# Performance work log

Hardware: AMD Instinct MI355X
Metric: run time of the kernel (lower is better)

## Reference

```python
import jax, jax.numpy as jnp
import numpy as np

N_ATOMS = 1_000_000
F_DIM = 128
H_DIM = 64
N_SPECIES = 4


def setup_inputs() -> dict:
    key = jax.random.key(0)
    ks = jax.random.split(key, 8)
    feats = jax.random.normal(ks[0], (N_ATOMS, F_DIM), dtype=jnp.float32)
    species = jax.random.randint(ks[1], (N_ATOMS,), 0, N_SPECIES, dtype=jnp.int64)
    # per-species MLP params, stacked on a leading species axis
    W1 = jax.random.normal(ks[2], (N_SPECIES, F_DIM, H_DIM), dtype=jnp.float32) / np.sqrt(F_DIM)
    b1 = jnp.zeros((N_SPECIES, H_DIM), dtype=jnp.float32)
    W2 = jax.random.normal(ks[3], (N_SPECIES, H_DIM, H_DIM), dtype=jnp.float32) / np.sqrt(H_DIM)
    b2 = jnp.zeros((N_SPECIES, H_DIM), dtype=jnp.float32)
    W3 = jax.random.normal(ks[4], (N_SPECIES, H_DIM, 1), dtype=jnp.float32) / np.sqrt(H_DIM)
    b3 = jnp.zeros((N_SPECIES, 1), dtype=jnp.float32)
    return {"features": feats, "species_indices": species,
            "W1": W1, "b1": b1, "W2": W2, "b2": b2, "W3": W3, "b3": b3}


def reference(features, species_indices, W1, b1, W2, b2, W3, b3):
    # Per-atom energy: dispatch each atom to its species' small tanh MLP.
    # Faithful to the torch mask-gather/scatter loop: we evaluate each
    # species MLP densely (n_species is tiny) and select per atom,
    # which computes identical outputs for the selected atoms.
    n_species = W1.shape[0]
    E = jnp.zeros((features.shape[0],), dtype=features.dtype)
    for s in range(n_species):
        h = jnp.tanh(features @ W1[s] + b1[s])   # [N, H]
        h = jnp.tanh(h @ W2[s] + b2[s])          # [N, H]
        e = (h @ W3[s] + b3[s])[:, 0]            # [N]
        E = jnp.where(species_indices == s, e, E)
    return E
```

## Files before the change

kernel.cpp:

```cpp
#include <hip/hip_runtime.h>

#define NSP 4

typedef unsigned short u16;
typedef __bf16 v8bf __attribute__((ext_vector_type(8)));
typedef float v4f __attribute__((ext_vector_type(4)));

__device__ __forceinline__ u16 f2bf(float f){
  union { float f; unsigned u; } v; v.f = f;
  unsigned u = v.u;
  u += 0x7fffu + ((u >> 16) & 1u);
  return (u16)(u >> 16);
}
__device__ __forceinline__ u16 h2bf(float f){
  union { float f; unsigned u; } v; v.f = f;
  return (u16)((v.u + 0x8000u) >> 16);
}
__device__ __forceinline__ unsigned pack2bf(float x, float y){
  union { float f; unsigned u; } a, b; a.f = x; b.f = y;
  unsigned ux = a.u + 0x8000u, uy = b.u + 0x8000u;
  return (uy & 0xffff0000u) | (ux >> 16);
}
__device__ __forceinline__ float fast_tanh(float x){
  float xc = fminf(fmaxf(x, -9.f), 9.f);
  float e = __expf(2.f * xc);
  return 1.f - 2.f * __builtin_amdgcn_rcpf(e + 1.f);
}


__global__ void init_k(int* __restrict__ counts2){
  counts2[threadIdx.x] = 0;
}

__global__ void hist_k(const int* __restrict__ sp, int n, int* __restrict__ counts2){
  int i = blockIdx.x * 256 + threadIdx.x;
  int sv = (i < n) ? sp[i] : -1;
  int b = blockIdx.x & 63;
  int lane = threadIdx.x & 63;
  #pragma unroll
  for (int s = 0; s < NSP; ++s){
    unsigned long long m = __ballot(sv == s);
    if (lane == 0 && m) atomicAdd(&counts2[s*64 + b], (int)__popcll(m));
  }
}

__global__ void scan_k(const int* __restrict__ counts2, int* __restrict__ cursors2,
                       int* __restrict__ segOff){
  __shared__ int tmp[256];
  int tid = threadIdx.x;
  int v = counts2[tid];
  tmp[tid] = v; __syncthreads();
  #pragma unroll
  for (int off = 1; off < 256; off <<= 1){
    int t = (tid >= off) ? tmp[tid - off] : 0;
    __syncthreads();
    tmp[tid] += t;
    __syncthreads();
  }
  int incl = tmp[tid];
  cursors2[tid] = incl - v;
  if ((tid & 63) == 0) segOff[tid >> 6] = incl - v;
  if (tid == 255)      segOff[NSP] = incl;
}

__global__ void scatter_k(const int* __restrict__ sp, int n,
                          int* __restrict__ cursors2, int* __restrict__ sorted){
  int i = blockIdx.x * 256 + threadIdx.x;
  int sv = (i < n) ? sp[i] : -1;
  int b = blockIdx.x & 63;
  int lane = threadIdx.x & 63;
  #pragma unroll
  for (int s = 0; s < NSP; ++s){
    unsigned long long m = __ballot(sv == s);
    if (!m) continue;
    int leader = __ffsll(m) - 1;
    int base = 0;
    if (lane == leader) base = atomicAdd(&cursors2[s*64 + b], (int)__popcll(m));
    base = __shfl(base, leader, 64);
    if (sv == s){
      int rank = (int)__popcll(m & ((1ull << lane) - 1ull));
      sorted[base + rank] = i;
    }
  }
}

__global__ void wconv_k(const float* __restrict__ W1, const float* __restrict__ W2,
                        u16* __restrict__ w1t, u16* __restrict__ w2t){
  int i = blockIdx.x * 256 + threadIdx.x;
  if (i < NSP*128*64){
    int s = i >> 13, rem = i & 8191, k = rem >> 6, nn = rem & 63;
    w1t[(s*64 + nn)*128 + k] = f2bf(W1[i]);
  }
  if (i < NSP*64*64){
    int s = i >> 12, rem = i & 4095, k = rem >> 6, nn = rem & 63;
    w2t[(s*64 + nn)*64 + k] = f2bf(W2[i]);
  }
}


#define BPS 128

__global__ __launch_bounds__(256, 2) void mlp2_k(
    const float* __restrict__ feats,
    const float* __restrict__ b1, const float* __restrict__ b2,
    const float* __restrict__ W3, const float* __restrict__ b3,
    const int* __restrict__ segOff, const int* __restrict__ sorted,
    const u16* __restrict__ w1t, const u16* __restrict__ w2t,
    float* __restrict__ out)
{
  __shared__ __align__(16) u16 sW1[64*136];
  __shared__ __align__(16) u16 sW2[64*72];
  __shared__ float sB1[64], sB2[64], sW3s[64];
  __shared__ __align__(16) u16 sH[4][16*72];

  int s  = blockIdx.x >> 7;
  int bs = blockIdx.x & (BPS-1);
  int tid = threadIdx.x;
  int segB = segOff[s], segE = segOff[s+1];
  int cnt = segE - segB;
  int tiles = (cnt + 63) >> 6;

  {
    int r = tid >> 2, q = tid & 3;
    const uint4* sp1 = (const uint4*)(w1t + (size_t)(s*64 + r)*128 + q*32);
    uint4 a0 = sp1[0], a1 = sp1[1], a2 = sp1[2], a3 = sp1[3];
    const uint4* sp2 = (const uint4*)(w2t + (size_t)(s*64 + r)*64 + q*16);
    uint4 c0 = sp2[0], c1 = sp2[1];
    uint4* d1 = (uint4*)(sW1 + r*136 + q*32);
    d1[0]=a0; d1[1]=a1; d1[2]=a2; d1[3]=a3;
    uint4* d2 = (uint4*)(sW2 + r*72 + q*16);
    d2[0]=c0; d2[1]=c1;
  }
  if (tid < 64)        sB1[tid]       = b1[s*64 + tid];
  else if (tid < 128)  sB2[tid-64]    = b2[s*64 + tid-64];
  else if (tid < 192)  sW3s[tid-128]  = W3[s*64 + tid-128];
  __syncthreads();

  int lane = tid & 63, wv = tid >> 6;
  int cc = lane & 15, quad = lane >> 4;

  v8bf bw1[4][4], bw2[4][2];
  float rb1[4], rb2[4], rw3[4];
  #pragma unroll
  for (int nt = 0; nt < 4; ++nt){
    #pragma unroll
    for (int kk = 0; kk < 4; ++kk)
      bw1[nt][kk] = *(const v8bf*)(sW1 + (nt*16+cc)*136 + kk*32 + quad*8);
    #pragma unroll
    for (int kk = 0; kk < 2; ++kk)
      bw2[nt][kk] = *(const v8bf*)(sW2 + (nt*16+cc)*72 + kk*32 + quad*8);
    rb1[nt] = sB1[nt*16+cc];
    rb2[nt] = sB2[nt*16+cc];
    rw3[nt] = sW3s[nt*16+cc];
  }
  float b3v = b3[s];
  u16* myH = sH[wv];

  if (tiles <= 0) return;

  auto idxLoad = [&](int t) -> int {
    int tc = t < tiles-1 ? t : tiles-1;
    int p = segB + tc*64 + wv*16 + cc;
    if (p > segE-1) p = segE-1;
    return sorted[p];
  };
  auto featLoad = [&](int ri, float4 (&f)[8]){
    const float4* fp = (const float4*)(feats + (size_t)ri*128 + quad*8);
    #pragma unroll
    for (int kk = 0; kk < 4; ++kk){ f[kk*2] = fp[kk*8]; f[kk*2+1] = fp[kk*8+1]; }
  };
  auto compute = [&](int t, const float4 (&f)[8], int ri){
    v4f acc[4];
    #pragma unroll
    for (int nt = 0; nt < 4; ++nt) acc[nt] = (v4f){0.f,0.f,0.f,0.f};
    #pragma unroll
    for (int kk = 0; kk < 4; ++kk){
      union { v8bf v; unsigned u[4]; } A;
      A.u[0] = pack2bf(f[kk*2].x,   f[kk*2].y);
      A.u[1] = pack2bf(f[kk*2].z,   f[kk*2].w);
      A.u[2] = pack2bf(f[kk*2+1].x, f[kk*2+1].y);
      A.u[3] = pack2bf(f[kk*2+1].z, f[kk*2+1].w);
      #pragma unroll
      for (int nt = 0; nt < 4; ++nt)
        acc[nt] = __builtin_amdgcn_mfma_f32_16x16x32_bf16(A.v, bw1[nt][kk], acc[nt], 0, 0, 0);
    }
    #pragma unroll
    for (int nt = 0; nt < 4; ++nt){
      #pragma unroll
      for (int r = 0; r < 4; ++r)
        myH[(quad*4+r)*72 + nt*16+cc] = h2bf(fast_tanh(acc[nt][r] + rb1[nt]));
    }
    v4f acc2[4];
    #pragma unroll
    for (int nt = 0; nt < 4; ++nt) acc2[nt] = (v4f){0.f,0.f,0.f,0.f};
    #pragma unroll
    for (int kk = 0; kk < 2; ++kk){
      v8bf hA = *(const v8bf*)(myH + cc*72 + kk*32 + quad*8);
      #pragma unroll
      for (int nt = 0; nt < 4; ++nt)
        acc2[nt] = __builtin_amdgcn_mfma_f32_16x16x32_bf16(hA, bw2[nt][kk], acc2[nt], 0, 0, 0);
    }
    float p[4] = {0.f,0.f,0.f,0.f};
    #pragma unroll
    for (int nt = 0; nt < 4; ++nt){
      #pragma unroll
      for (int r = 0; r < 4; ++r)
        p[r] += fast_tanh(acc2[nt][r] + rb2[nt]) * rw3[nt];
    }
    #pragma unroll
    for (int off = 8; off >= 1; off >>= 1){
      #pragma unroll
      for (int r = 0; r < 4; ++r) p[r] += __shfl_xor(p[r], off, 64);
    }
    int rid[4];
    #pragma unroll
    for (int r = 0; r < 4; ++r) rid[r] = __shfl(ri, quad*4 + r, 64);
    if (cc == 0){
      int atomBase = t*64 + wv*16;
      #pragma unroll
      for (int r = 0; r < 4; ++r){
        int ap = atomBase + quad*4 + r;
        if (ap < cnt) out[rid[r]] = p[r] + b3v;
      }
    }
  };

  int t0 = bs;
  int riA = idxLoad(t0);
  int riB = idxLoad(t0 + BPS);
  float4 fA[8];
  featLoad(riA, fA);
  for (int t = t0; t < tiles; t += BPS){
    int riC = idxLoad(t + 2*BPS);
    float4 fB[8];
    featLoad(riB, fB);
    compute(t, fA, riA);
    riA = riB; riB = riC;
    #pragma unroll
    for (int i = 0; i < 8; ++i) fA[i] = fB[i];
  }
}

extern "C" void kernel_launch(void* const* d_in, const int* in_sizes, int n_in,
                              void* d_out, int out_size, void* d_ws, size_t ws_size,
                              hipStream_t stream){
  const float* feats  = (const float*)d_in[0];
  const int*   species= (const int*)d_in[1];
  const float* W1 = (const float*)d_in[2];
  const float* b1 = (const float*)d_in[3];
  const float* W2 = (const float*)d_in[4];
  const float* b2 = (const float*)d_in[5];
  const float* W3 = (const float*)d_in[6];
  const float* b3 = (const float*)d_in[7];
  float* out = (float*)d_out;
  int n = in_sizes[1];

  char* ws = (char*)d_ws;
  int* counts2  = (int*)ws;
  int* cursors2 = (int*)(ws + 1024);
  int* segOff   = (int*)(ws + 2048);
  int* sorted   = (int*)(ws + 4096);
  size_t sortedBytes = ((size_t)n*4 + 15) & ~(size_t)15;
  u16* w1t = (u16*)(ws + 4096 + sortedBytes);
  u16* w2t = w1t + NSP*64*128;

  int nb = (n + 255) / 256;
  init_k<<<1, 256, 0, stream>>>(counts2);
  hist_k<<<nb, 256, 0, stream>>>(species, n, counts2);
  wconv_k<<<(NSP*128*64 + 255)/256, 256, 0, stream>>>(W1, W2, w1t, w2t);
  scan_k<<<1, 256, 0, stream>>>(counts2, cursors2, segOff);
  scatter_k<<<nb, 256, 0, stream>>>(species, n, cursors2, sorted);
  mlp2_k<<<NSP*BPS, 256, 0, stream>>>(feats, b1, b2, W3, b3, segOff, sorted, w1t, w2t, out);
}
```

Baseline: 870.0 us.

## Restructure species sort pipeline and MLP kernel with transposed MFMA operands

Weight conversion is merged into the histogram kernel. The atomic-based per-slot counters are replaced by per-block histograms, a single-block 1024-thread scan and an atomic-free stable scatter, so atoms stay in index order within each species. The MLP kernel now puts the weights in the A operand of the MFMA, so each lane ends with one atom's energy and only two shuffles are needed for the reduction. It also writes the hidden layer to LDS with packed stores, converts the next tile's features to bf16 ahead of time, and gives each block a contiguous range of tiles instead of a strided one. The tanh clamp is dropped, which relies on exp overflow and underflow still giving ±1.

```diff
diff --git a/kernel.cpp b/kernel.cpp
--- a/kernel.cpp
+++ b/kernel.cpp
@@ -12,95 +12,119 @@
   u += 0x7fffu + ((u >> 16) & 1u);
   return (u16)(u >> 16);
 }
-__device__ __forceinline__ u16 h2bf(float f){
-  union { float f; unsigned u; } v; v.f = f;
-  return (u16)((v.u + 0x8000u) >> 16);
-}
 __device__ __forceinline__ unsigned pack2bf(float x, float y){
   union { float f; unsigned u; } a, b; a.f = x; b.f = y;
   unsigned ux = a.u + 0x8000u, uy = b.u + 0x8000u;
   return (uy & 0xffff0000u) | (ux >> 16);
 }
 __device__ __forceinline__ float fast_tanh(float x){
-  float xc = fminf(fmaxf(x, -9.f), 9.f);
-  float e = __expf(2.f * xc);
+  float e = __expf(2.f * x);
   return 1.f - 2.f * __builtin_amdgcn_rcpf(e + 1.f);
 }
 
-
-__global__ void init_k(int* __restrict__ counts2){
-  counts2[threadIdx.x] = 0;
-}
-
-__global__ void hist_k(const int* __restrict__ sp, int n, int* __restrict__ counts2){
-  int i = blockIdx.x * 256 + threadIdx.x;
+__global__ void histwconv_k(const int* __restrict__ sp, int n, int nb,
+                            int* __restrict__ hist,
+                            const float* __restrict__ W1, const float* __restrict__ W2,
+                            u16* __restrict__ w1t, u16* __restrict__ w2t){
+  int blk = blockIdx.x, tid = threadIdx.x;
+  if (blk >= nb){
+    int i = (blk - nb)*256 + tid;
+    if (i < NSP*128*64){
+      int s = i >> 13, rem = i & 8191, k = rem >> 6, nn = rem & 63;
+      w1t[(s*64 + nn)*128 + k] = f2bf(W1[i]);
+    }
+    if (i < NSP*64*64){
+      int s = i >> 12, rem = i & 4095, k = rem >> 6, nn = rem & 63;
+      w2t[(s*64 + nn)*64 + k] = f2bf(W2[i]);
+    }
+    return;
+  }
+  int i = blk*256 + tid;
   int sv = (i < n) ? sp[i] : -1;
-  int b = blockIdx.x & 63;
-  int lane = threadIdx.x & 63;
+  __shared__ int wc[4][NSP];
+  int lane = tid & 63, wv = tid >> 6;
   #pragma unroll
   for (int s = 0; s < NSP; ++s){
     unsigned long long m = __ballot(sv == s);
-    if (lane == 0 && m) atomicAdd(&counts2[s*64 + b], (int)__popcll(m));
-  }
-}
-
-__global__ void scan_k(const int* __restrict__ counts2, int* __restrict__ cursors2,
-                       int* __restrict__ segOff){
-  __shared__ int tmp[256];
+    if (lane == 0) wc[wv][s] = (int)__popcll(m);
+  }
+  __syncthreads();
+  if (tid < NSP)
+    hist[tid*nb + blk] = wc[0][tid] + wc[1][tid] + wc[2][tid] + wc[3][tid];
+}
+
+__global__ __launch_bounds__(1024) void scan_k2(const int* __restrict__ hist, int nb,
+                                                int* __restrict__ base, int* __restrict__ segOff){
+  int total = NSP*nb;
   int tid = threadIdx.x;
-  int v = counts2[tid];
-  tmp[tid] = v; __syncthreads();
-  #pragma unroll
-  for (int off = 1; off < 256; off <<= 1){
-    int t = (tid >= off) ? tmp[tid - off] : 0;
-    __syncthreads();
-    tmp[tid] += t;
-    __syncthreads();
-  }
-  int incl = tmp[tid];
-  cursors2[tid] = incl - v;
-  if ((tid & 63) == 0) segOff[tid >> 6] = incl - v;
-  if (tid == 255)      segOff[NSP] = incl;
-}
-
-__global__ void scatter_k(const int* __restrict__ sp, int n,
-                          int* __restrict__ cursors2, int* __restrict__ sorted){
-  int i = blockIdx.x * 256 + threadIdx.x;
+  int g0 = tid*16;
+  int v[16]; int s = 0;
+  #pragma unroll
+  for (int i = 0; i < 16; ++i){
+    int g = g0 + i;
+    int x = (g < total) ? hist[g] : 0;
+    v[i] = s; s += x;
+  }
+  int lane = tid & 63, wv = tid >> 6;
+  int incl = s;
+  #pragma unroll
+  for (int off = 1; off < 64; off <<= 1){
+    int t = __shfl_up(incl, off, 64);
+    if (lane >= off) incl += t;
+  }
+  __shared__ int wsum[16];
+  if (lane == 63) wsum[wv] = incl;
+  __syncthreads();
+  int wbase = 0;
+  #pragma unroll
+  for (int w = 0; w < 16; ++w) wbase += (w < wv) ? wsum[w] : 0;
+  int exclT = wbase + incl - s;
+  #pragma unroll
+  for (int i = 0; i < 16; ++i){
+    int g = g0 + i;
+    int e = exclT + v[i];
+    if (g < total) base[g] = e;
+    if (g <= total && (g % nb) == 0) segOff[g / nb] = e;
+  }
+}
+
+__global__ void scatter_k2(const int* __restrict__ sp, int n, int nb,
+                           const int* __restrict__ base, int* __restrict__ sorted){
+  int blk = blockIdx.x, tid = threadIdx.x;
+  int i = blk*256 + tid;
   int sv = (i < n) ? sp[i] : -1;
-  int b = blockIdx.x & 63;
-  int lane = threadIdx.x & 63;
+  __shared__ int cnt[4][NSP];
+  __shared__ int wb[4][NSP];
+  __shared__ int hb[NSP];
+  int lane = tid & 63, wv = tid >> 6;
+  unsigned long long msel = 0;
   #pragma unroll
   for (int s = 0; s < NSP; ++s){
     unsigned long long m = __ballot(sv == s);
-    if (!m) continue;
-    int leader = __ffsll(m) - 1;
-    int base = 0;
-    if (lane == leader) base = atomicAdd(&cursors2[s*64 + b], (int)__popcll(m));
-    base = __shfl(base, leader, 64);
-    if (sv == s){
-      int rank = (int)__popcll(m & ((1ull << lane) - 1ull));
-      sorted[base + rank] = i;
-    }
-  }
-}
-
-__global__ void wconv_k(const float* __restrict__ W1, const float* __restrict__ W2,
-                        u16* __restrict__ w1t, u16* __restrict__ w2t){
-  int i = blockIdx.x * 256 + threadIdx.x;
-  if (i < NSP*128*64){
-    int s = i >> 13, rem = i & 8191, k = rem >> 6, nn = rem & 63;
-    w1t[(s*64 + nn)*128 + k] = f2bf(W1[i]);
-  }
-  if (i < NSP*64*64){
-    int s = i >> 12, rem = i & 4095, k = rem >> 6, nn = rem & 63;
-    w2t[(s*64 + nn)*64 + k] = f2bf(W2[i]);
+    if (lane == 0) cnt[wv][s] = (int)__popcll(m);
+    if (sv == s) msel = m;
+  }
+  if (tid < NSP) hb[tid] = base[tid*nb + blk];
+  __syncthreads();
+  if (tid < 16){
+    int w = tid >> 2, s = tid & 3;
+    int b = hb[s];
+    if (w > 0) b += cnt[0][s];
+    if (w > 1) b += cnt[1][s];
+    if (w > 2) b += cnt[2][s];
+    wb[w][s] = b;
+  }
+  __syncthreads();
+  if (sv >= 0){
+    int rank = (int)__popcll(msel & ((1ull << lane) - 1ull));
+    sorted[wb[wv][sv] + rank] = i;
   }
 }
 
 
 #define BPS 128
 
-__global__ __launch_bounds__(256, 2) void mlp2_k(
+__global__ __launch_bounds__(256, 2) void mlp3_k(
     const float* __restrict__ feats,
     const float* __restrict__ b1, const float* __restrict__ b2,
     const float* __restrict__ W3, const float* __restrict__ b3,
@@ -140,7 +164,7 @@
   int cc = lane & 15, quad = lane >> 4;
 
   v8bf bw1[4][4], bw2[4][2];
-  float rb1[4], rb2[4], rw3[4];
+  float b1c[4][4], b2c[4][4], w3c[4][4];
   #pragma unroll
   for (int nt = 0; nt < 4; ++nt){
     #pragma unroll
@@ -149,17 +173,23 @@
     #pragma unroll
     for (int kk = 0; kk < 2; ++kk)
       bw2[nt][kk] = *(const v8bf*)(sW2 + (nt*16+cc)*72 + kk*32 + quad*8);
-    rb1[nt] = sB1[nt*16+cc];
-    rb2[nt] = sB2[nt*16+cc];
-    rw3[nt] = sW3s[nt*16+cc];
+    #pragma unroll
+    for (int r = 0; r < 4; ++r){
+      b1c[nt][r] = sB1[nt*16 + quad*4 + r];
+      b2c[nt][r] = sB2[nt*16 + quad*4 + r];
+      w3c[nt][r] = sW3s[nt*16 + quad*4 + r];
+    }
   }
   float b3v = b3[s];
-  u16* myH = sH[wv];
-
-  if (tiles <= 0) return;
+  u16* myH = (u16*)sH[wv];
+
+  int per = (tiles + BPS - 1) >> 7;
+  int tBeg = bs * per;
+  int tEnd = min(tiles, tBeg + per);
+  if (tBeg >= tEnd) return;
 
   auto idxLoad = [&](int t) -> int {
-    int tc = t < tiles-1 ? t : tiles-1;
+    int tc = t < tEnd-1 ? t : tEnd-1;
     int p = segB + tc*64 + wv*16 + cc;
     if (p > segE-1) p = segE-1;
     return sorted[p];
@@ -169,75 +199,69 @@
     #pragma unroll
     for (int kk = 0; kk < 4; ++kk){ f[kk*2] = fp[kk*8]; f[kk*2+1] = fp[kk*8+1]; }
   };
-  auto compute = [&](int t, const float4 (&f)[8], int ri){
+  auto packA = [&](const float4 (&f)[8], unsigned (&P)[4][4]){
+    #pragma unroll
+    for (int kk = 0; kk < 4; ++kk){
+      P[kk][0] = pack2bf(f[kk*2].x,   f[kk*2].y);
+      P[kk][1] = pack2bf(f[kk*2].z,   f[kk*2].w);
+      P[kk][2] = pack2bf(f[kk*2+1].x, f[kk*2+1].y);
+      P[kk][3] = pack2bf(f[kk*2+1].z, f[kk*2+1].w);
+    }
+  };
+
+  auto compute = [&](int t, const unsigned (&P)[4][4], int ri){
     v4f acc[4];
     #pragma unroll
     for (int nt = 0; nt < 4; ++nt) acc[nt] = (v4f){0.f,0.f,0.f,0.f};
     #pragma unroll
     for (int kk = 0; kk < 4; ++kk){
-      union { v8bf v; unsigned u[4]; } A;
-      A.u[0] = pack2bf(f[kk*2].x,   f[kk*2].y);
-      A.u[1] = pack2bf(f[kk*2].z,   f[kk*2].w);
-      A.u[2] = pack2bf(f[kk*2+1].x, f[kk*2+1].y);
-      A.u[3] = pack2bf(f[kk*2+1].z, f[kk*2+1].w);
+      union { v8bf v; unsigned u[4]; } B;
+      B.u[0] = P[kk][0]; B.u[1] = P[kk][1]; B.u[2] = P[kk][2]; B.u[3] = P[kk][3];
       #pragma unroll
       for (int nt = 0; nt < 4; ++nt)
-        acc[nt] = __builtin_amdgcn_mfma_f32_16x16x32_bf16(A.v, bw1[nt][kk], acc[nt], 0, 0, 0);
+        acc[nt] = __builtin_amdgcn_mfma_f32_16x16x32_bf16(bw1[nt][kk], B.v, acc[nt], 0, 0, 0);
     }
     #pragma unroll
     for (int nt = 0; nt < 4; ++nt){
+      float t0 = fast_tanh(acc[nt][0] + b1c[nt][0]);
+      float t1 = fast_tanh(acc[nt][1] + b1c[nt][1]);
+      float t2 = fast_tanh(acc[nt][2] + b1c[nt][2]);
+      float t3 = fast_tanh(acc[nt][3] + b1c[nt][3]);
+      uint2 w; w.x = pack2bf(t0, t1); w.y = pack2bf(t2, t3);
+      *(uint2*)(myH + cc*72 + nt*16 + quad*4) = w;
+    }
+    v8bf hB0 = *(const v8bf*)(myH + cc*72 +  0 + quad*8);
+    v8bf hB1 = *(const v8bf*)(myH + cc*72 + 32 + quad*8);
+    float e = 0.f;
+    #pragma unroll
+    for (int nt = 0; nt < 4; ++nt){
+      v4f a2 = (v4f){0.f,0.f,0.f,0.f};
+      a2 = __builtin_amdgcn_mfma_f32_16x16x32_bf16(bw2[nt][0], hB0, a2, 0, 0, 0);
+      a2 = __builtin_amdgcn_mfma_f32_16x16x32_bf16(bw2[nt][1], hB1, a2, 0, 0, 0);
       #pragma unroll
       for (int r = 0; r < 4; ++r)
-        myH[(quad*4+r)*72 + nt*16+cc] = h2bf(fast_tanh(acc[nt][r] + rb1[nt]));
-    }
-    v4f acc2[4];
-    #pragma unroll
-    for (int nt = 0; nt < 4; ++nt) acc2[nt] = (v4f){0.f,0.f,0.f,0.f};
-    #pragma unroll
-    for (int kk = 0; kk < 2; ++kk){
-      v8bf hA = *(const v8bf*)(myH + cc*72 + kk*32 + quad*8);
-      #pragma unroll
-      for (int nt = 0; nt < 4; ++nt)
-        acc2[nt] = __builtin_amdgcn_mfma_f32_16x16x32_bf16(hA, bw2[nt][kk], acc2[nt], 0, 0, 0);
-    }
-    float p[4] = {0.f,0.f,0.f,0.f};
-    #pragma unroll
-    for (int nt = 0; nt < 4; ++nt){
-      #pragma unroll
-      for (int r = 0; r < 4; ++r)
-        p[r] += fast_tanh(acc2[nt][r] + rb2[nt]) * rw3[nt];
-    }
-    #pragma unroll
-    for (int off = 8; off >= 1; off >>= 1){
-      #pragma unroll
-      for (int r = 0; r < 4; ++r) p[r] += __shfl_xor(p[r], off, 64);
-    }
-    int rid[4];
-    #pragma unroll
-    for (int r = 0; r < 4; ++r) rid[r] = __shfl(ri, quad*4 + r, 64);
-    if (cc == 0){
-      int atomBase = t*64 + wv*16;
-      #pragma unroll
-      for (int r = 0; r < 4; ++r){
-        int ap = atomBase + quad*4 + r;
-        if (ap < cnt) out[rid[r]] = p[r] + b3v;
-      }
-    }
-  };
-
-  int t0 = bs;
-  int riA = idxLoad(t0);
-  int riB = idxLoad(t0 + BPS);
-  float4 fA[8];
-  featLoad(riA, fA);
-  for (int t = t0; t < tiles; t += BPS){
-    int riC = idxLoad(t + 2*BPS);
-    float4 fB[8];
-    featLoad(riB, fB);
-    compute(t, fA, riA);
+        e += fast_tanh(a2[r] + b2c[nt][r]) * w3c[nt][r];
+    }
+    e += __shfl_xor(e, 16, 64);
+    e += __shfl_xor(e, 32, 64);
+    if (quad == 0){
+      int ap = t*64 + wv*16 + cc;
+      if (ap < cnt) out[ri] = e + b3v;
+    }
+  };
+
+  int riA = idxLoad(tBeg);
+  int riB = idxLoad(tBeg + 1);
+  float4 fR[8];
+  unsigned PA[4][4];
+  featLoad(riA, fR);
+  packA(fR, PA);
+  for (int t = tBeg; t < tEnd; ++t){
+    int riC = idxLoad(t + 2);
+    featLoad(riB, fR);
+    compute(t, PA, riA);
+    packA(fR, PA);
     riA = riB; riB = riC;
-    #pragma unroll
-    for (int i = 0; i < 8; ++i) fA[i] = fB[i];
   }
 }
 
@@ -254,21 +278,20 @@
   const float* b3 = (const float*)d_in[7];
   float* out = (float*)d_out;
   int n = in_sizes[1];
+  int nb = (n + 255) / 256;
 
   char* ws = (char*)d_ws;
-  int* counts2  = (int*)ws;
-  int* cursors2 = (int*)(ws + 1024);
-  int* segOff   = (int*)(ws + 2048);
-  int* sorted   = (int*)(ws + 4096);
-  size_t sortedBytes = ((size_t)n*4 + 15) & ~(size_t)15;
-  u16* w1t = (u16*)(ws + 4096 + sortedBytes);
+  size_t histB = ((size_t)NSP*nb*4 + 15) & ~(size_t)15;
+  int* hist   = (int*)ws;
+  int* base   = (int*)(ws + histB);
+  int* segOff = (int*)(ws + 2*histB);
+  int* sorted = (int*)(ws + 2*histB + 32);
+  size_t sortedB = ((size_t)n*4 + 15) & ~(size_t)15;
+  u16* w1t = (u16*)(ws + 2*histB + 32 + sortedB);
   u16* w2t = w1t + NSP*64*128;
 
-  int nb = (n + 255) / 256;
-  init_k<<<1, 256, 0, stream>>>(counts2);
-  hist_k<<<nb, 256, 0, stream>>>(species, n, counts2);
-  wconv_k<<<(NSP*128*64 + 255)/256, 256, 0, stream>>>(W1, W2, w1t, w2t);
-  scan_k<<<1, 256, 0, stream>>>(counts2, cursors2, segOff);
-  scatter_k<<<nb, 256, 0, stream>>>(species, n, cursors2, sorted);
-  mlp2_k<<<NSP*BPS, 256, 0, stream>>>(feats, b1, b2, W3, b3, segOff, sorted, w1t, w2t, out);
-}
+  histwconv_k<<<nb + 128, 256, 0, stream>>>(species, n, nb, hist, W1, W2, w1t, w2t);
+  scan_k2<<<1, 1024, 0, stream>>>(hist, nb, base, segOff);
+  scatter_k2<<<nb, 256, 0, stream>>>(species, n, nb, base, sorted);
+  mlp3_k<<<NSP*BPS, 256, 0, stream>>>(feats, b1, b2, W3, b3, segOff, sorted, w1t, w2t, out);
+}
```

New measurement: 700.1 us. -19.5%, faster.
